# Kernel optimization log

Measured on AMD Instinct MI355X. Metric: run time of the kernel, lower is better.

## Reference

```python
import jax, jax.numpy as jnp
import numpy as np

N_NODES = 100000
N_EDGES = 1600000
IN_F = 256
OUT_F = 64
ALPHA = 0.2  # LeakyReLU negative slope


def setup_inputs() -> dict:
    key = jax.random.key(0)
    k1, k2, k3, k4 = jax.random.split(key, 4)
    x = jax.random.normal(k1, (N_NODES, IN_F), dtype=jnp.float32)
    indices = jax.random.randint(k2, (2, N_EDGES), 0, N_NODES, dtype=jnp.int64)
    # xavier_uniform with gain=1.414 ~ U(-b, b), b = gain*sqrt(6/(fan_in+fan_out))
    bW = 1.414 * np.sqrt(6.0 / (IN_F + OUT_F))
    W = jax.random.uniform(k3, (IN_F, OUT_F), dtype=jnp.float32, minval=-bW, maxval=bW)
    ba = 1.414 * np.sqrt(6.0 / (2 * OUT_F + 1))
    a = jax.random.uniform(k4, (2 * OUT_F, 1), dtype=jnp.float32, minval=-ba, maxval=ba)
    return {"x": x, "indices": indices, "W": W, "a": a}


def reference(x, indices, W, a):
    # h = X @ W  -> [N, F_out]
    h = x @ W
    N = h.shape[0]
    src = indices[0]  # segment ids (softmax rows / aggregation targets)
    dst = indices[1]  # gathered neighbor features

    # e_ij = leakyrelu([h_i || h_j] @ a) = leakyrelu(h_i@a1 + h_j@a2)
    # (identical math to concatenation, avoids materializing [E, 2F])
    a1 = a[:OUT_F, 0]
    a2 = a[OUT_F:, 0]
    s1 = h @ a1  # [N]
    s2 = h @ a2  # [N]
    logits = s1[src] + s2[dst]  # [E]
    e = jnp.where(logits > 0, logits, ALPHA * logits)

    # segment softmax over edges grouped by src (sp_softmax)
    m = jax.ops.segment_max(e, src, num_segments=N)
    ex = jnp.exp(e - m[src])
    denom = jax.ops.segment_sum(ex, src, num_segments=N)
    att = ex / denom[src]  # [E]

    # h_prime[i] = sum_j att_ij * h_j  (sp_matmul: weighted scatter-aggregate)
    h_prime = jax.ops.segment_sum(att[:, None] * h[dst], src, num_segments=N)

    # concat=True -> ELU
    return jax.nn.elu(h_prime)
```

## Files before the change

kernel.cpp:

```cpp
#include <hip/hip_runtime.h>
#include <hip/hip_bf16.h>
#include <math.h>

#define NN 100000
#define NE 1600000
#define INF_ 256
#define OF 64

#define NPB 128
#define NB  782
#define CAPB 2560
#define ED (CAPB + 128)
#define GEMMB 782
#define P1B 512
#define CH1 ((NE + P1B - 1) / P1B)
#define OVCAP 8192

constexpr float LRELU_ALPHA = 0.2f;

typedef __attribute__((ext_vector_type(8))) short short8;
typedef __attribute__((ext_vector_type(4))) float f32x4;

static __device__ __forceinline__ unsigned short f2bf(float f) {
    union { float f; unsigned int u; } v; v.f = f;
    unsigned int r = v.u + 0x7fff + ((v.u >> 16) & 1);
    return (unsigned short)(r >> 16);
}
static __device__ __forceinline__ float bf2f(unsigned short b) {
    union { unsigned int u; float f; } v; v.u = ((unsigned int)b) << 16;
    return v.f;
}
static __device__ __forceinline__ unsigned int pkbf(float a, float b) {
    union { __hip_bfloat162 h; unsigned int u; } c;
    c.h = __float22bfloat162_rn(make_float2(a, b));
    return c.u;
}

union S8 { short8 s; unsigned int u[4]; };

__global__ __launch_bounds__(256) void k_prep(const float* __restrict__ W,
                                              const float* __restrict__ a,
                                              float* __restrict__ wa) {
    int r = threadIdx.x;
    float t1 = 0.f, t2 = 0.f;
#pragma unroll 8
    for (int c = 0; c < OF; ++c) {
        float w = W[r * OF + c];
        t1 += w * a[c];
        t2 += w * a[OF + c];
    }
    wa[r] = t1;
    wa[256 + r] = t2;
}

__global__ __launch_bounds__(256, 3) void k_fused1(const float* __restrict__ x,
                                                   const float* __restrict__ W,
                                                   const float* __restrict__ wa,
                                                   const int* __restrict__ idx,
                                                   int* __restrict__ cur_b,
                                                   int* __restrict__ pairs,
                                                   int2* __restrict__ ov_list,
                                                   unsigned short* __restrict__ h,
                                                   float* __restrict__ s1,
                                                   float* __restrict__ s2) {
    __shared__ __align__(16) char smem[32768];
    int tid = threadIdx.x;

    if (blockIdx.x < GEMMB) {
        short* Wf = (short*)smem;
        for (int i = tid; i < 2048; i += 256) {
            int ks = i >> 8;
            int ct = (i >> 6) & 3;
            int l  = i & 63;
            int kb = ks * 32 + ((l >> 4) << 3);
            int col = ct * 16 + (l & 15);
            S8 v;
#pragma unroll
            for (int j = 0; j < 4; ++j)
                v.u[j] = pkbf(W[(size_t)(kb + 2 * j) * OF + col],
                              W[(size_t)(kb + 2 * j + 1) * OF + col]);
            ((short8*)Wf)[i] = v.s;
        }

        int wid = tid >> 6, lane = tid & 63;
        int rowbase = blockIdx.x * 128 + wid * 32;
        int c = lane & 15;
        int koff = (lane >> 4) << 3;

        short8 frag5[8];
        {
#pragma unroll
            for (int ks = 0; ks < 8; ++ks) {
                S8 v;
                if (c < 2) {
                    const float* src = wa + c * 256 + ks * 32 + koff;
                    float4 u0 = *(const float4*)src;
                    float4 u1 = *(const float4*)(src + 4);
                    v.u[0] = pkbf(u0.x, u0.y); v.u[1] = pkbf(u0.z, u0.w);
                    v.u[2] = pkbf(u1.x, u1.y); v.u[3] = pkbf(u1.z, u1.w);
                } else {
                    v.u[0] = 0u; v.u[1] = 0u; v.u[2] = 0u; v.u[3] = 0u;
                }
                frag5[ks] = v.s;
            }
        }
        __syncthreads();

        int r0 = rowbase + c;
        int rc0 = min(r0, NN - 1);
        int rc1 = min(r0 + 16, NN - 1);
        const float* p0 = x + (size_t)rc0 * INF_ + koff;
        const float* p1 = x + (size_t)rc1 * INF_ + koff;

        f32x4 acc[2][5];
#pragma unroll
        for (int rt = 0; rt < 2; ++rt)
#pragma unroll
            for (int ct = 0; ct < 5; ++ct) acc[rt][ct] = (f32x4){0.f, 0.f, 0.f, 0.f};

#pragma unroll
        for (int ks = 0; ks < 8; ++ks) {
            float4 xa0 = *(const float4*)(p0 + ks * 32);
            float4 xb0 = *(const float4*)(p0 + ks * 32 + 4);
            float4 xa1 = *(const float4*)(p1 + ks * 32);
            float4 xb1 = *(const float4*)(p1 + ks * 32 + 4);
            S8 af[2];
            af[0].u[0] = pkbf(xa0.x, xa0.y); af[0].u[1] = pkbf(xa0.z, xa0.w);
            af[0].u[2] = pkbf(xb0.x, xb0.y); af[0].u[3] = pkbf(xb0.z, xb0.w);
            af[1].u[0] = pkbf(xa1.x, xa1.y); af[1].u[1] = pkbf(xa1.z, xa1.w);
            af[1].u[2] = pkbf(xb1.x, xb1.y); af[1].u[3] = pkbf(xb1.z, xb1.w);
#pragma unroll
            for (int rt = 0; rt < 2; ++rt) {
#pragma unroll
                for (int ct = 0; ct < 4; ++ct)
                    acc[rt][ct] = __builtin_amdgcn_mfma_f32_16x16x32_bf16(
                        af[rt].s, ((short8*)Wf)[(ks * 4 + ct) * 64 + lane], acc[rt][ct], 0, 0, 0);
                acc[rt][4] = __builtin_amdgcn_mfma_f32_16x16x32_bf16(
                    af[rt].s, frag5[ks], acc[rt][4], 0, 0, 0);
            }
        }

        int rowq = lane >> 4;
#pragma unroll
        for (int rt = 0; rt < 2; ++rt) {
#pragma unroll
            for (int reg = 0; reg < 4; ++reg) {
                int r = rowbase + rt * 16 + rowq * 4 + reg;
                if (r < NN) {
#pragma unroll
                    for (int ct = 0; ct < 4; ++ct)
                        h[(size_t)r * OF + ct * 16 + c] = f2bf(acc[rt][ct][reg]);
                    float sv = acc[rt][4][reg];
                    if (c == 0)      s1[r] = sv;
                    else if (c == 1) s2[r] = sv;
                }
            }
        }
    } else {
        int blk = blockIdx.x - GEMMB;
        int* hist  = (int*)smem;
        int* gbase = (int*)smem + NB;
        for (int i = tid; i < NB; i += 256) hist[i] = 0;
        __syncthreads();
        int e0 = blk * CH1, e1 = min(e0 + CH1, NE);
        for (int e = e0 + tid; e < e1; e += 256)
            atomicAdd(&hist[idx[e] >> 7], 1);
        __syncthreads();
        for (int i = tid; i < NB; i += 256) {
            int cc = hist[i];
            gbase[i] = cc ? atomicAdd(&cur_b[i], cc) : 0;
            hist[i] = 0;
        }
        __syncthreads();
        for (int e = e0 + tid; e < e1; e += 256) {
            int s = idx[e], d = idx[NE + e];
            int b = s >> 7;
            int p = gbase[b] + atomicAdd(&hist[b], 1);
            if (p < CAPB) pairs[b * CAPB + p] = ((s & 127) << 17) | d;
            else {
                int j = atomicAdd(&cur_b[NB], 1);
                if (j < OVCAP) ov_list[j] = make_int2(s, d);
            }
        }
    }
}

__global__ __launch_bounds__(256) void k_part2(const int* __restrict__ pairs,
                                               const int* __restrict__ cur_b,
                                               const int2* __restrict__ ov_list,
                                               const float* __restrict__ s1,
                                               const float* __restrict__ s2,
                                               int* __restrict__ start,
                                               int* __restrict__ deg,
                                               int2* __restrict__ el_g) {
    __shared__ int stage[ED];
    __shared__ int cnt[NPB], pfx[NPB], cur[NPB];
    __shared__ float s1l[NPB];
    __shared__ int extra;
    int tid = threadIdx.x, b = blockIdx.x;
    int node0 = b * NPB;

    if (tid < NPB) {
        cnt[tid] = 0;
        int g = node0 + tid;
        s1l[tid] = (g < NN) ? s1[g] : 0.f;
    }
    if (tid == 0) extra = 0;
    __syncthreads();

    int t_b = cur_b[b];
    int nin = min(t_b, CAPB);
    for (int i = tid; i < nin; i += 256) {
        int v = pairs[b * CAPB + i];
        stage[i] = v;
        atomicAdd(&cnt[v >> 17], 1);
    }
    if (t_b > CAPB) {
        int ovn = min(cur_b[NB], OVCAP);
        for (int i = tid; i < ovn; i += 256) {
            int2 e = ov_list[i];
            if ((e.x >> 7) == b) {
                int k = atomicAdd(&extra, 1);
                if (k < 128) {
                    stage[CAPB + k] = ((e.x & 127) << 17) | e.y;
                    atomicAdd(&cnt[e.x & 127], 1);
                }
            }
        }
    }
    __syncthreads();
    int ntot = nin + min(extra, 128);

    if (tid < NPB) pfx[tid] = cnt[tid];
    __syncthreads();
    for (int off = 1; off < NPB; off <<= 1) {
        int xv = (tid >= off && tid < NPB) ? pfx[tid - off] : 0;
        __syncthreads();
        if (tid < NPB) pfx[tid] += xv;
        __syncthreads();
    }
    if (tid < NPB) {
        int ex = pfx[tid] - cnt[tid];
        int g = node0 + tid;
        if (g < NN) { start[g] = b * CAPB + ex; deg[g] = cnt[tid]; }
        cur[tid] = ex;
    }
    __syncthreads();
    for (int i = tid; i < ntot; i += 256) {
        int v = stage[i];
        int ls = v >> 17, dst = v & 0x1FFFF;
        int p = atomicAdd(&cur[ls], 1);
        float lg = s1l[ls] + s2[dst];
        float elr = lg > 0.f ? lg : LRELU_ALPHA * lg;
        el_g[b * CAPB + p] = make_int2(dst, __float_as_int(expf(elr)));
    }
}

__global__ __launch_bounds__(256) void k_agg(const int2* __restrict__ el_g,
                                             const int* __restrict__ start,
                                             const int* __restrict__ deg,
                                             const unsigned short* __restrict__ h,
                                             float* __restrict__ out) {
    __shared__ int2 tile[4][64];
    int tid = threadIdx.x;
    int wid = tid >> 6, lane = tid & 63;
    int node = blockIdx.x * 4 + wid;
    if (node >= NN) return;

    int st = start[node];
    int dg = deg[node];
    int half = lane >> 5, f2 = lane & 31;
    float den = 0.f, ax = 0.f, ay = 0.f;

    for (int base = 0; base < dg; base += 64) {
        int cnt = min(64, dg - base);
        if (lane < cnt) {
            int2 pr = el_g[st + base + lane];
            den += __int_as_float(pr.y);
            tile[wid][lane] = pr;
        }
        asm volatile("s_waitcnt lgkmcnt(0)" ::: "memory");
#pragma unroll 4
        for (int j = half; j < cnt; j += 2) {
            int2 e = tile[wid][j];
            float ex = __int_as_float(e.y);
            unsigned int hv = *(const unsigned int*)(h + (size_t)e.x * OF + f2 * 2);
            ax += ex * bf2f((unsigned short)(hv & 0xFFFFu));
            ay += ex * bf2f((unsigned short)(hv >> 16));
        }
        asm volatile("" ::: "memory");
    }

#pragma unroll
    for (int off = 1; off < 64; off <<= 1) den += __shfl_xor(den, off, 64);
    ax += __shfl_xor(ax, 32, 64);
    ay += __shfl_xor(ay, 32, 64);

    float inv = den > 0.f ? 1.f / den : 0.f;
    float vx = ax * inv, vy = ay * inv;
    vx = vx > 0.f ? vx : expf(vx) - 1.f;
    vy = vy > 0.f ? vy : expf(vy) - 1.f;
    if (half == 0)
        *(float2*)(out + (size_t)node * OF + f2 * 2) = make_float2(vx, vy);
}

extern "C" void kernel_launch(void* const* d_in, const int* in_sizes, int n_in,
                              void* d_out, int out_size, void* d_ws, size_t ws_size,
                              hipStream_t stream) {
    const float* x   = (const float*)d_in[0];
    const int*   idx = (const int*)d_in[1];
    const float* W   = (const float*)d_in[2];
    const float* a   = (const float*)d_in[3];
    float* out = (float*)d_out;

    char* ws = (char*)d_ws;
    unsigned short* h = (unsigned short*)ws;  ws += sizeof(unsigned short) * (size_t)NN * OF;
    int*  pairs       = (int*)ws;             ws += sizeof(int) * (size_t)NB * CAPB;
    int2* el_g        = (int2*)ws;            ws += sizeof(int2) * (size_t)NB * CAPB;
    float* s1         = (float*)ws;           ws += sizeof(float) * NN;
    float* s2         = (float*)ws;           ws += sizeof(float) * NN;
    int*   start      = (int*)ws;             ws += sizeof(int) * NN;
    int*   deg        = (int*)ws;             ws += sizeof(int) * NN;
    int*   cur_b      = (int*)ws;             ws += sizeof(int) * (NB + 16);
    int2*  ov_list    = (int2*)ws;            ws += sizeof(int2) * OVCAP;
    float* wa         = (float*)ws;           ws += sizeof(float) * 512;

    hipMemsetAsync(cur_b, 0, sizeof(int) * (NB + 16), stream);
    k_prep<<<1, 256, 0, stream>>>(W, a, wa);
    k_fused1<<<GEMMB + P1B, 256, 0, stream>>>(x, W, wa, idx, cur_b, pairs, ov_list, h, s1, s2);
    k_part2<<<NB, 256, 0, stream>>>(pairs, cur_b, ov_list, s1, s2, start, deg, el_g);
    k_agg<<<(NN + 3) / 4, 256, 0, stream>>>(el_g, start, deg, h, out);
}
```

Before: 288.8 us.

## Fold W·a prep into fused GEMM kernel and use 512-thread blocks

Removes the separate single-block k_prep launch. Each GEMM block now computes the W·a vectors itself into shared memory. The fused kernel moves to 512 threads per block, with each wave computing 16 rows instead of 32, and the partition path is adjusted to the larger stride. This drops one kernel launch and its serialization in exchange for redundant per-block W·a work (782 blocks × 256×64 FMAs) and lower per-wave MFMA reuse of the shared W fragments.

New measurement: 278.8 us. 1.04x faster.

```diff
diff --git a/kernel.cpp b/kernel.cpp
--- a/kernel.cpp
+++ b/kernel.cpp
@@ -38,24 +38,9 @@
 
 union S8 { short8 s; unsigned int u[4]; };
 
-__global__ __launch_bounds__(256) void k_prep(const float* __restrict__ W,
-                                              const float* __restrict__ a,
-                                              float* __restrict__ wa) {
-    int r = threadIdx.x;
-    float t1 = 0.f, t2 = 0.f;
-#pragma unroll 8
-    for (int c = 0; c < OF; ++c) {
-        float w = W[r * OF + c];
-        t1 += w * a[c];
-        t2 += w * a[OF + c];
-    }
-    wa[r] = t1;
-    wa[256 + r] = t2;
-}
-
-__global__ __launch_bounds__(256, 3) void k_fused1(const float* __restrict__ x,
+__global__ __launch_bounds__(512, 6) void k_fused1(const float* __restrict__ x,
                                                    const float* __restrict__ W,
-                                                   const float* __restrict__ wa,
+                                                   const float* __restrict__ a,
                                                    const int* __restrict__ idx,
                                                    int* __restrict__ cur_b,
                                                    int* __restrict__ pairs,
@@ -63,12 +48,26 @@
                                                    unsigned short* __restrict__ h,
                                                    float* __restrict__ s1,
                                                    float* __restrict__ s2) {
-    __shared__ __align__(16) char smem[32768];
+    __shared__ __align__(16) char smem[34816];
     int tid = threadIdx.x;
 
     if (blockIdx.x < GEMMB) {
-        short* Wf = (short*)smem;
-        for (int i = tid; i < 2048; i += 256) {
+        short* Wf  = (short*)smem;
+        float* wal = (float*)(smem + 32768);
+
+        if (tid < 256) {
+            float t1 = 0.f, t2 = 0.f;
+            const float* wr = W + tid * OF;
+#pragma unroll 8
+            for (int cc = 0; cc < OF; ++cc) {
+                float w = wr[cc];
+                t1 += w * a[cc];
+                t2 += w * a[OF + cc];
+            }
+            wal[tid] = t1;
+            wal[256 + tid] = t2;
+        }
+        for (int i = tid; i < 2048; i += 512) {
             int ks = i >> 8;
             int ct = (i >> 6) & 3;
             int l  = i & 63;
@@ -81,98 +80,80 @@
                               W[(size_t)(kb + 2 * j + 1) * OF + col]);
             ((short8*)Wf)[i] = v.s;
         }
+        __syncthreads();
 
         int wid = tid >> 6, lane = tid & 63;
-        int rowbase = blockIdx.x * 128 + wid * 32;
+        int rowbase = blockIdx.x * 128 + wid * 16;
         int c = lane & 15;
         int koff = (lane >> 4) << 3;
 
         short8 frag5[8];
-        {
-#pragma unroll
-            for (int ks = 0; ks < 8; ++ks) {
-                S8 v;
-                if (c < 2) {
-                    const float* src = wa + c * 256 + ks * 32 + koff;
-                    float4 u0 = *(const float4*)src;
-                    float4 u1 = *(const float4*)(src + 4);
-                    v.u[0] = pkbf(u0.x, u0.y); v.u[1] = pkbf(u0.z, u0.w);
-                    v.u[2] = pkbf(u1.x, u1.y); v.u[3] = pkbf(u1.z, u1.w);
-                } else {
-                    v.u[0] = 0u; v.u[1] = 0u; v.u[2] = 0u; v.u[3] = 0u;
-                }
-                frag5[ks] = v.s;
-            }
-        }
-        __syncthreads();
+#pragma unroll
+        for (int ks = 0; ks < 8; ++ks) {
+            S8 v;
+            if (c < 2) {
+                const float* src = wal + c * 256 + ks * 32 + koff;
+                v.u[0] = pkbf(src[0], src[1]); v.u[1] = pkbf(src[2], src[3]);
+                v.u[2] = pkbf(src[4], src[5]); v.u[3] = pkbf(src[6], src[7]);
+            } else {
+                v.u[0] = 0u; v.u[1] = 0u; v.u[2] = 0u; v.u[3] = 0u;
+            }
+            frag5[ks] = v.s;
+        }
 
         int r0 = rowbase + c;
         int rc0 = min(r0, NN - 1);
-        int rc1 = min(r0 + 16, NN - 1);
         const float* p0 = x + (size_t)rc0 * INF_ + koff;
-        const float* p1 = x + (size_t)rc1 * INF_ + koff;
-
-        f32x4 acc[2][5];
-#pragma unroll
-        for (int rt = 0; rt < 2; ++rt)
-#pragma unroll
-            for (int ct = 0; ct < 5; ++ct) acc[rt][ct] = (f32x4){0.f, 0.f, 0.f, 0.f};
+
+        f32x4 acc[5];
+#pragma unroll
+        for (int ct = 0; ct < 5; ++ct) acc[ct] = (f32x4){0.f, 0.f, 0.f, 0.f};
 
 #pragma unroll
         for (int ks = 0; ks < 8; ++ks) {
-            float4 xa0 = *(const float4*)(p0 + ks * 32);
-            float4 xb0 = *(const float4*)(p0 + ks * 32 + 4);
-            float4 xa1 = *(const float4*)(p1 + ks * 32);
-            float4 xb1 = *(const float4*)(p1 + ks * 32 + 4);
-            S8 af[2];
-            af[0].u[0] = pkbf(xa0.x, xa0.y); af[0].u[1] = pkbf(xa0.z, xa0.w);
-            af[0].u[2] = pkbf(xb0.x, xb0.y); af[0].u[3] = pkbf(xb0.z, xb0.w);
-            af[1].u[0] = pkbf(xa1.x, xa1.y); af[1].u[1] = pkbf(xa1.z, xa1.w);
-            af[1].u[2] = pkbf(xb1.x, xb1.y); af[1].u[3] = pkbf(xb1.z, xb1.w);
-#pragma unroll
-            for (int rt = 0; rt < 2; ++rt) {
+            float4 xa = *(const float4*)(p0 + ks * 32);
+            float4 xb = *(const float4*)(p0 + ks * 32 + 4);
+            S8 af;
+            af.u[0] = pkbf(xa.x, xa.y); af.u[1] = pkbf(xa.z, xa.w);
+            af.u[2] = pkbf(xb.x, xb.y); af.u[3] = pkbf(xb.z, xb.w);
+#pragma unroll
+            for (int ct = 0; ct < 4; ++ct)
+                acc[ct] = __builtin_amdgcn_mfma_f32_16x16x32_bf16(
+                    af.s, ((short8*)Wf)[(ks * 4 + ct) * 64 + lane], acc[ct], 0, 0, 0);
+            acc[4] = __builtin_amdgcn_mfma_f32_16x16x32_bf16(
+                af.s, frag5[ks], acc[4], 0, 0, 0);
+        }
+
+        int rowq = lane >> 4;
+#pragma unroll
+        for (int reg = 0; reg < 4; ++reg) {
+            int r = rowbase + rowq * 4 + reg;
+            if (r < NN) {
 #pragma unroll
                 for (int ct = 0; ct < 4; ++ct)
-                    acc[rt][ct] = __builtin_amdgcn_mfma_f32_16x16x32_bf16(
-                        af[rt].s, ((short8*)Wf)[(ks * 4 + ct) * 64 + lane], acc[rt][ct], 0, 0, 0);
-                acc[rt][4] = __builtin_amdgcn_mfma_f32_16x16x32_bf16(
-                    af[rt].s, frag5[ks], acc[rt][4], 0, 0, 0);
-            }
-        }
-
-        int rowq = lane >> 4;
-#pragma unroll
-        for (int rt = 0; rt < 2; ++rt) {
-#pragma unroll
-            for (int reg = 0; reg < 4; ++reg) {
-                int r = rowbase + rt * 16 + rowq * 4 + reg;
-                if (r < NN) {
-#pragma unroll
-                    for (int ct = 0; ct < 4; ++ct)
-                        h[(size_t)r * OF + ct * 16 + c] = f2bf(acc[rt][ct][reg]);
-                    float sv = acc[rt][4][reg];
-                    if (c == 0)      s1[r] = sv;
-                    else if (c == 1) s2[r] = sv;
-                }
+                    h[(size_t)r * OF + ct * 16 + c] = f2bf(acc[ct][reg]);
+                float sv = acc[4][reg];
+                if (c == 0)      s1[r] = sv;
+                else if (c == 1) s2[r] = sv;
             }
         }
     } else {
         int blk = blockIdx.x - GEMMB;
         int* hist  = (int*)smem;
         int* gbase = (int*)smem + NB;
-        for (int i = tid; i < NB; i += 256) hist[i] = 0;
+        for (int i = tid; i < NB; i += 512) hist[i] = 0;
         __syncthreads();
         int e0 = blk * CH1, e1 = min(e0 + CH1, NE);
-        for (int e = e0 + tid; e < e1; e += 256)
+        for (int e = e0 + tid; e < e1; e += 512)
             atomicAdd(&hist[idx[e] >> 7], 1);
         __syncthreads();
-        for (int i = tid; i < NB; i += 256) {
+        for (int i = tid; i < NB; i += 512) {
             int cc = hist[i];
             gbase[i] = cc ? atomicAdd(&cur_b[i], cc) : 0;
             hist[i] = 0;
         }
         __syncthreads();
-        for (int e = e0 + tid; e < e1; e += 256) {
+        for (int e = e0 + tid; e < e1; e += 512) {
             int s = idx[e], d = idx[NE + e];
             int b = s >> 7;
             int p = gbase[b] + atomicAdd(&hist[b], 1);
@@ -323,11 +304,9 @@
     int*   deg        = (int*)ws;             ws += sizeof(int) * NN;
     int*   cur_b      = (int*)ws;             ws += sizeof(int) * (NB + 16);
     int2*  ov_list    = (int2*)ws;            ws += sizeof(int2) * OVCAP;
-    float* wa         = (float*)ws;           ws += sizeof(float) * 512;
 
     hipMemsetAsync(cur_b, 0, sizeof(int) * (NB + 16), stream);
-    k_prep<<<1, 256, 0, stream>>>(W, a, wa);
-    k_fused1<<<GEMMB + P1B, 256, 0, stream>>>(x, W, wa, idx, cur_b, pairs, ov_list, h, s1, s2);
+    k_fused1<<<GEMMB + P1B, 512, 0, stream>>>(x, W, a, idx, cur_b, pairs, ov_list, h, s1, s2);
     k_part2<<<NB, 256, 0, stream>>>(pairs, cur_b, ov_list, s1, s2, start, deg, el_g);
     k_agg<<<(NN + 3) / 4, 256, 0, stream>>>(el_g, start, deg, h, out);
 }
```
